# Optimization experiments

Hardware: AMD Instinct MI355X
Metric: run time of the kernel (lower is better)

The kernel has to match this reference:

```python
import jax, jax.numpy as jnp
import numpy as np

B, D, C = 16384, 1024, 2048

def setup_inputs() -> dict:
    key = jax.random.key(0)
    k1, k2 = jax.random.split(key)
    x = jax.random.normal(k1, (B, D), dtype=jnp.float32)
    # kaiming_normal_ with nonlinearity='relu': std = sqrt(2 / fan_in)
    W = jax.random.normal(k2, (C, D), dtype=jnp.float32) * jnp.sqrt(2.0 / D)
    return {"x": x, "W": W, "task_id": 0}

def reference(x, W, task_id):
    # Original: -(x[:, :, None] - W.T[None, :, :])**2 .mean(1)  -> [B, C]
    # Algebraic rewrite: -(||x||^2/D - 2*x.W^T/D + ||w||^2/D)
    d = jnp.asarray(x.shape[1], x.dtype)
    x2 = jnp.sum(x * x, axis=1, keepdims=True) / d          # [B, 1]
    w2 = jnp.sum(W * W, axis=1) / d                          # [C]
    cross = jnp.einsum('bd,cd->bc', x, W) * (2.0 / d)        # [B, C]
    return cross - x2 - w2[None, :]
```

## Files before the change

kernel.cpp:

```cpp
#include <hip/hip_runtime.h>
#include <hip/hip_bf16.h>
#include <stdint.h>

#define B_ROWS 16384
#define D_DIM  1024
#define C_DIM  2048
#define MT_TOT (B_ROWS / 16)
#define NT_TOT (C_DIM  / 16)
#define KT_TOT (D_DIM  / 32)

typedef short bf16x8 __attribute__((ext_vector_type(8)));
typedef float f32x4  __attribute__((ext_vector_type(4)));

__global__ __launch_bounds__(256) void pack_norm(
        const float* __restrict__ x, const float* __restrict__ W,
        ushort* __restrict__ Apk, ushort* __restrict__ Bpk,
        float* __restrict__ x2, float* __restrict__ w2) {
    int chunk = blockIdx.x * 4 + (threadIdx.x >> 6);
    const int lane = threadIdx.x & 63;
    const int XCH = MT_TOT * KT_TOT;
    const float* src; ushort* dst; float* norm;
    if (chunk < XCH) { src = x; dst = Apk; norm = x2; }
    else             { src = W; dst = Bpk; norm = w2; chunk -= XCH; }
    const int tile = chunk >> 5;
    const int kt   = chunk & 31;

    const int row = tile * 16 + (lane & 15);
    const int k0  = kt * 32 + (lane >> 4) * 8;
    const float4 v0 = *(const float4*)(src + (size_t)row * D_DIM + k0);
    const float4 v1 = *(const float4*)(src + (size_t)row * D_DIM + k0 + 4);
    float s = v0.x*v0.x + v0.y*v0.y + v0.z*v0.z + v0.w*v0.w
            + v1.x*v1.x + v1.y*v1.y + v1.z*v1.z + v1.w*v1.w;

    ushort u[8]; __hip_bfloat16 h;
    h = __float2bfloat16(v0.x); u[0] = *(const ushort*)&h;
    h = __float2bfloat16(v0.y); u[1] = *(const ushort*)&h;
    h = __float2bfloat16(v0.z); u[2] = *(const ushort*)&h;
    h = __float2bfloat16(v0.w); u[3] = *(const ushort*)&h;
    h = __float2bfloat16(v1.x); u[4] = *(const ushort*)&h;
    h = __float2bfloat16(v1.y); u[5] = *(const ushort*)&h;
    h = __float2bfloat16(v1.z); u[6] = *(const ushort*)&h;
    h = __float2bfloat16(v1.w); u[7] = *(const ushort*)&h;
    *(bf16x8*)(dst + ((size_t)chunk * 64 + lane) * 8) = *(const bf16x8*)u;

    s += __shfl_xor(s, 16, 64);
    s += __shfl_xor(s, 32, 64);
    if (lane < 16) atomicAdd(norm + tile * 16 + lane, s * (1.0f / (float)D_DIM));
}

__global__ __launch_bounds__(256, 3) void gemm_pklds(
        const ushort* __restrict__ Apk, const ushort* __restrict__ Bpk,
        const float* __restrict__ x2, const float* __restrict__ w2,
        float* __restrict__ out) {
    __shared__ ushort As[16 * 512];
    __shared__ ushort Bs[16 * 512];

    const int tid  = threadIdx.x;
    const int lane = tid & 63;
    const int wv   = tid >> 6;

    const int wid = (blockIdx.x & 7) * 256 + (blockIdx.x >> 3);
    const int bm  = wid >> 4;
    const int bn  = wid & 15;

    const ushort* aSrc = Apk + ((size_t)(bm * 8) * KT_TOT) * 512 + lane * 8;
    const ushort* bSrc = Bpk + ((size_t)(bn * 8) * KT_TOT) * 512 + lane * 8;

    const ushort* aRd = As + (wv >> 1) * 4 * 1024 + lane * 8;
    const ushort* bRd = Bs + (wv & 1) * 4 * 1024 + lane * 8;

    f32x4 acc[4][4];
    #pragma unroll
    for (int mi = 0; mi < 4; ++mi)
        #pragma unroll
        for (int ni = 0; ni < 4; ++ni)
            acc[mi][ni] = (f32x4){0.f, 0.f, 0.f, 0.f};

    for (int kt = 0; kt < KT_TOT; kt += 2) {
        if (wv < 2) {
            #pragma unroll
            for (int r = 0; r < 8; ++r) {
                const int c    = wv * 8 + r;
                const int tile = c >> 1, ks = c & 1;
                __builtin_amdgcn_global_load_lds(
                    (const __attribute__((address_space(1))) void*)(
                        aSrc + ((size_t)tile * KT_TOT + kt + ks) * 512),
                    (__attribute__((address_space(3))) void*)(As + c * 512), 16, 0, 0);
            }
        } else {
            #pragma unroll
            for (int r = 0; r < 8; ++r) {
                const int c    = (wv - 2) * 8 + r;
                const int tile = c >> 1, ks = c & 1;
                __builtin_amdgcn_global_load_lds(
                    (const __attribute__((address_space(1))) void*)(
                        bSrc + ((size_t)tile * KT_TOT + kt + ks) * 512),
                    (__attribute__((address_space(3))) void*)(Bs + c * 512), 16, 0, 0);
            }
        }
        __syncthreads();

        #pragma unroll
        for (int ks = 0; ks < 2; ++ks) {
            bf16x8 a[4], b[4];
            #pragma unroll
            for (int mi = 0; mi < 4; ++mi)
                a[mi] = *(const bf16x8*)(aRd + mi * 1024 + ks * 512);
            #pragma unroll
            for (int ni = 0; ni < 4; ++ni)
                b[ni] = *(const bf16x8*)(bRd + ni * 1024 + ks * 512);
            #pragma unroll
            for (int mi = 0; mi < 4; ++mi)
                #pragma unroll
                for (int ni = 0; ni < 4; ++ni)
                    acc[mi][ni] = __builtin_amdgcn_mfma_f32_16x16x32_bf16(
                        a[mi], b[ni], acc[mi][ni], 0, 0, 0);
        }
        __syncthreads();
    }

    const float scale = 2.0f / (float)D_DIM;
    const int rsel = lane & 15;
    const int quad = lane >> 4;
    const int mT0  = bm * 8 + (wv >> 1) * 4;
    const int nT0  = bn * 8 + (wv & 1) * 4;
    const int row0 = mT0 * 16 + quad * 4;
    const int col0 = nT0 * 16 + rsel;

    float x2r[4][4];
    #pragma unroll
    for (int mi = 0; mi < 4; ++mi)
        #pragma unroll
        for (int r = 0; r < 4; ++r)
            x2r[mi][r] = x2[row0 + mi * 16 + r];

    #pragma unroll
    for (int ni = 0; ni < 4; ++ni) {
        const int c = col0 + ni * 16;
        const float wc = w2[c];
        #pragma unroll
        for (int mi = 0; mi < 4; ++mi) {
            #pragma unroll
            for (int r = 0; r < 4; ++r) {
                const int rr = row0 + mi * 16 + r;
                out[(size_t)rr * C_DIM + c] = acc[mi][ni][r] * scale - x2r[mi][r] - wc;
            }
        }
    }
}

extern "C" void kernel_launch(void* const* d_in, const int* in_sizes, int n_in,
                              void* d_out, int out_size, void* d_ws, size_t ws_size,
                              hipStream_t stream) {
    const float* x = (const float*)d_in[0];
    const float* W = (const float*)d_in[1];
    float* out = (float*)d_out;

    char* ws = (char*)d_ws;
    ushort* Apk = (ushort*)ws;
    ushort* Bpk = (ushort*)(ws + (size_t)B_ROWS * D_DIM * sizeof(ushort));
    float*  x2  = (float*)(ws + (size_t)(B_ROWS + C_DIM) * D_DIM * sizeof(ushort));
    float*  w2  = x2 + B_ROWS;

    hipMemsetAsync(x2, 0, (B_ROWS + C_DIM) * sizeof(float), stream);

    pack_norm<<<(MT_TOT * KT_TOT + NT_TOT * KT_TOT) / 4, 256, 0, stream>>>(
        x, W, Apk, Bpk, x2, w2);

    gemm_pklds<<<(B_ROWS / 128) * (C_DIM / 128), 256, 0, stream>>>(
        Apk, Bpk, x2, w2, out);
}
```

Measured before the change: 255.1 us.

## Rewrite GEMM as 256x256-tile, 8-wave kernel with phased double-buffered LDS pipeline

Replaces the 128x128-tile, 4-wave GEMM with a 256x256-tile, 512-thread kernel. Each wave now computes a 128x64 sub-tile. The K loop is split into four phases that interleave global-to-LDS prefetch of the next K slices with MFMA work on the current buffer. It uses explicit vmcnt waits, raw barriers and s_setprio to keep matrix instructions flowing. This aims to raise data reuse per LDS byte and hide memory latency, at the cost of more registers (32 accumulators per wave), 128KB of LDS and fragile hand-placed synchronisation.

Result: slower. 272.1 us (+6.6%).

```diff
diff --git a/kernel.cpp b/kernel.cpp
--- a/kernel.cpp
+++ b/kernel.cpp
@@ -5,12 +5,21 @@
 #define B_ROWS 16384
 #define D_DIM  1024
 #define C_DIM  2048
+#define KT32   (D_DIM / 32)
+#define KT     (D_DIM / 64)
 #define MT_TOT (B_ROWS / 16)
 #define NT_TOT (C_DIM  / 16)
-#define KT_TOT (D_DIM  / 32)
 
 typedef short bf16x8 __attribute__((ext_vector_type(8)));
 typedef float f32x4  __attribute__((ext_vector_type(4)));
+
+#define AS1 __attribute__((address_space(1)))
+#define AS3 __attribute__((address_space(3)))
+#define BARRIER __builtin_amdgcn_s_barrier()
+#define LGKM0 asm volatile("s_waitcnt lgkmcnt(0)")
+#define VMCNT(n) asm volatile("s_waitcnt vmcnt(" #n ")" ::: "memory")
+#define PRIO1 __builtin_amdgcn_s_setprio(1)
+#define PRIO0 __builtin_amdgcn_s_setprio(0)
 
 __global__ __launch_bounds__(256) void pack_norm(
         const float* __restrict__ x, const float* __restrict__ W,
@@ -18,7 +27,7 @@
         float* __restrict__ x2, float* __restrict__ w2) {
     int chunk = blockIdx.x * 4 + (threadIdx.x >> 6);
     const int lane = threadIdx.x & 63;
-    const int XCH = MT_TOT * KT_TOT;
+    const int XCH = MT_TOT * KT32;
     const float* src; ushort* dst; float* norm;
     if (chunk < XCH) { src = x; dst = Apk; norm = x2; }
     else             { src = W; dst = Bpk; norm = w2; chunk -= XCH; }
@@ -48,105 +57,131 @@
     if (lane < 16) atomicAdd(norm + tile * 16 + lane, s * (1.0f / (float)D_DIM));
 }
 
-__global__ __launch_bounds__(256, 3) void gemm_pklds(
+__global__ __launch_bounds__(512, 2) void gemm_8ph(
         const ushort* __restrict__ Apk, const ushort* __restrict__ Bpk,
         const float* __restrict__ x2, const float* __restrict__ w2,
         float* __restrict__ out) {
-    __shared__ ushort As[16 * 512];
-    __shared__ ushort Bs[16 * 512];
+    __shared__ ushort As[32768];
+    __shared__ ushort Bs[32768];
 
     const int tid  = threadIdx.x;
     const int lane = tid & 63;
     const int wv   = tid >> 6;
-
-    const int wid = (blockIdx.x & 7) * 256 + (blockIdx.x >> 3);
-    const int bm  = wid >> 4;
-    const int bn  = wid & 15;
-
-    const ushort* aSrc = Apk + ((size_t)(bm * 8) * KT_TOT) * 512 + lane * 8;
-    const ushort* bSrc = Bpk + ((size_t)(bn * 8) * KT_TOT) * 512 + lane * 8;
-
-    const ushort* aRd = As + (wv >> 1) * 4 * 1024 + lane * 8;
-    const ushort* bRd = Bs + (wv & 1) * 4 * 1024 + lane * 8;
-
-    f32x4 acc[4][4];
+    const int wm   = wv >> 2;
+    const int wn   = wv & 3;
+
+    const int wid = (blockIdx.x & 7) * 64 + (blockIdx.x >> 3);
+    const int bm  = wid >> 3;
+    const int bn  = wid & 7;
+
+    const ushort* aSrc = Apk + (size_t)bm * 16 * KT32 * 512 + lane * 8;
+    const ushort* bSrc = Bpk + (size_t)bn * 16 * KT32 * 512 + lane * 8;
+    const ushort* aRd  = As + wm * 8192 + lane * 8;
+    const ushort* bRd  = Bs + wn * 4096 + lane * 8;
+
+    const int mt0 = wv * 2, mt1 = wv * 2 + 1;
+
+#define STA(mt, ktc, ldsOff) __builtin_amdgcn_global_load_lds( \
+        (const AS1 void*)(aSrc + ((size_t)(mt) * KT32 + (ktc)) * 512), \
+        (AS3 void*)(As + (ldsOff)), 16, 0, 0)
+#define STB(nt, ktc, ldsOff) __builtin_amdgcn_global_load_lds( \
+        (const AS1 void*)(bSrc + ((size_t)(nt) * KT32 + (ktc)) * 512), \
+        (AS3 void*)(Bs + (ldsOff)), 16, 0, 0)
+#define LDA(bo, mi, ks) (*(const bf16x8*)(aRd + (bo) + (mi) * 1024 + (ks) * 512))
+#define LDB(bo, ni, ks) (*(const bf16x8*)(bRd + (bo) + (ni) * 1024 + (ks) * 512))
+#define MFMA4(av, mi) \
+    acc[mi][0] = __builtin_amdgcn_mfma_f32_16x16x32_bf16(av, b0, acc[mi][0], 0, 0, 0); \
+    acc[mi][1] = __builtin_amdgcn_mfma_f32_16x16x32_bf16(av, b1, acc[mi][1], 0, 0, 0); \
+    acc[mi][2] = __builtin_amdgcn_mfma_f32_16x16x32_bf16(av, b2, acc[mi][2], 0, 0, 0); \
+    acc[mi][3] = __builtin_amdgcn_mfma_f32_16x16x32_bf16(av, b3, acc[mi][3], 0, 0, 0)
+
+    f32x4 acc[8][4];
     #pragma unroll
-    for (int mi = 0; mi < 4; ++mi)
+    for (int mi = 0; mi < 8; ++mi)
         #pragma unroll
         for (int ni = 0; ni < 4; ++ni)
             acc[mi][ni] = (f32x4){0.f, 0.f, 0.f, 0.f};
 
-    for (int kt = 0; kt < KT_TOT; kt += 2) {
-        if (wv < 2) {
-            #pragma unroll
-            for (int r = 0; r < 8; ++r) {
-                const int c    = wv * 8 + r;
-                const int tile = c >> 1, ks = c & 1;
-                __builtin_amdgcn_global_load_lds(
-                    (const __attribute__((address_space(1))) void*)(
-                        aSrc + ((size_t)tile * KT_TOT + kt + ks) * 512),
-                    (__attribute__((address_space(3))) void*)(As + c * 512), 16, 0, 0);
-            }
-        } else {
-            #pragma unroll
-            for (int r = 0; r < 8; ++r) {
-                const int c    = (wv - 2) * 8 + r;
-                const int tile = c >> 1, ks = c & 1;
-                __builtin_amdgcn_global_load_lds(
-                    (const __attribute__((address_space(1))) void*)(
-                        bSrc + ((size_t)tile * KT_TOT + kt + ks) * 512),
-                    (__attribute__((address_space(3))) void*)(Bs + c * 512), 16, 0, 0);
-            }
-        }
-        __syncthreads();
-
-        #pragma unroll
-        for (int ks = 0; ks < 2; ++ks) {
-            bf16x8 a[4], b[4];
-            #pragma unroll
-            for (int mi = 0; mi < 4; ++mi)
-                a[mi] = *(const bf16x8*)(aRd + mi * 1024 + ks * 512);
-            #pragma unroll
-            for (int ni = 0; ni < 4; ++ni)
-                b[ni] = *(const bf16x8*)(bRd + ni * 1024 + ks * 512);
-            #pragma unroll
-            for (int mi = 0; mi < 4; ++mi)
-                #pragma unroll
-                for (int ni = 0; ni < 4; ++ni)
-                    acc[mi][ni] = __builtin_amdgcn_mfma_f32_16x16x32_bf16(
-                        a[mi], b[ni], acc[mi][ni], 0, 0, 0);
-        }
-        __syncthreads();
+    STA(mt0, 0, mt0 * 1024);              STA(mt1, 0, mt1 * 1024);
+    STB(mt0, 0, mt0 * 1024);              STB(mt1, 0, mt1 * 1024);
+    STA(mt0, 1, mt0 * 1024 + 512);        STA(mt1, 1, mt1 * 1024 + 512);
+    STB(mt0, 1, mt0 * 1024 + 512);        STB(mt1, 1, mt1 * 1024 + 512);
+    STA(mt0, 2, 16384 + mt0 * 1024);      STA(mt1, 2, 16384 + mt1 * 1024);
+    STB(mt0, 2, 16384 + mt0 * 1024);      STB(mt1, 2, 16384 + mt1 * 1024);
+    VMCNT(8);
+    BARRIER;
+
+    #pragma unroll 2
+    for (int kt = 0; kt < KT; ++kt) {
+        const int bo  = (kt & 1) * 16384;
+        const int nbo = bo ^ 16384;
+        const int kc1 = ((kt + 1) * 2 + 1) & 31;
+        const int kc2 = ((kt + 2) * 2) & 31;
+        bf16x8 a0, a1, a2, a3, b0, b1, b2, b3;
+
+        b0 = LDB(bo, 0, 0); b1 = LDB(bo, 1, 0); b2 = LDB(bo, 2, 0); b3 = LDB(bo, 3, 0);
+        a0 = LDA(bo, 0, 0); a1 = LDA(bo, 1, 0); a2 = LDA(bo, 2, 0); a3 = LDA(bo, 3, 0);
+        STA(mt0, kc1, nbo + mt0 * 1024 + 512);
+        STA(mt1, kc1, nbo + mt1 * 1024 + 512);
+        BARRIER; LGKM0; PRIO1;
+        MFMA4(a0, 0); MFMA4(a1, 1); MFMA4(a2, 2); MFMA4(a3, 3);
+        PRIO0; BARRIER;
+
+        a0 = LDA(bo, 4, 0); a1 = LDA(bo, 5, 0); a2 = LDA(bo, 6, 0); a3 = LDA(bo, 7, 0);
+        STB(mt0, kc1, nbo + mt0 * 1024 + 512);
+        STB(mt1, kc1, nbo + mt1 * 1024 + 512);
+        VMCNT(8);
+        BARRIER; LGKM0; PRIO1;
+        MFMA4(a0, 4); MFMA4(a1, 5); MFMA4(a2, 6); MFMA4(a3, 7);
+        PRIO0; BARRIER;
+
+        b0 = LDB(bo, 0, 1); b1 = LDB(bo, 1, 1); b2 = LDB(bo, 2, 1); b3 = LDB(bo, 3, 1);
+        a0 = LDA(bo, 0, 1); a1 = LDA(bo, 1, 1); a2 = LDA(bo, 2, 1); a3 = LDA(bo, 3, 1);
+        STA(mt0, kc2, bo + mt0 * 1024);
+        STA(mt1, kc2, bo + mt1 * 1024);
+        BARRIER; LGKM0; PRIO1;
+        MFMA4(a0, 0); MFMA4(a1, 1); MFMA4(a2, 2); MFMA4(a3, 3);
+        PRIO0; BARRIER;
+
+        a0 = LDA(bo, 4, 1); a1 = LDA(bo, 5, 1); a2 = LDA(bo, 6, 1); a3 = LDA(bo, 7, 1);
+        STB(mt0, kc2, bo + mt0 * 1024);
+        STB(mt1, kc2, bo + mt1 * 1024);
+        VMCNT(8);
+        BARRIER; LGKM0; PRIO1;
+        MFMA4(a0, 4); MFMA4(a1, 5); MFMA4(a2, 6); MFMA4(a3, 7);
+        PRIO0; BARRIER;
     }
 
     const float scale = 2.0f / (float)D_DIM;
     const int rsel = lane & 15;
     const int quad = lane >> 4;
-    const int mT0  = bm * 8 + (wv >> 1) * 4;
-    const int nT0  = bn * 8 + (wv & 1) * 4;
-    const int row0 = mT0 * 16 + quad * 4;
-    const int col0 = nT0 * 16 + rsel;
-
-    float x2r[4][4];
+    const int row0 = bm * 256 + wm * 128 + quad * 4;
+    const int col0 = bn * 256 + wn * 64 + rsel;
+
+    float w2c[4];
     #pragma unroll
-    for (int mi = 0; mi < 4; ++mi)
+    for (int ni = 0; ni < 4; ++ni) w2c[ni] = w2[col0 + ni * 16];
+
+    #pragma unroll
+    for (int mi = 0; mi < 8; ++mi) {
+        const int rbase = row0 + mi * 16;
+        float xr[4];
         #pragma unroll
-        for (int r = 0; r < 4; ++r)
-            x2r[mi][r] = x2[row0 + mi * 16 + r];
-
-    #pragma unroll
-    for (int ni = 0; ni < 4; ++ni) {
-        const int c = col0 + ni * 16;
-        const float wc = w2[c];
+        for (int r = 0; r < 4; ++r) xr[r] = x2[rbase + r];
         #pragma unroll
-        for (int mi = 0; mi < 4; ++mi) {
+        for (int ni = 0; ni < 4; ++ni) {
+            const int c = col0 + ni * 16;
             #pragma unroll
-            for (int r = 0; r < 4; ++r) {
-                const int rr = row0 + mi * 16 + r;
-                out[(size_t)rr * C_DIM + c] = acc[mi][ni][r] * scale - x2r[mi][r] - wc;
-            }
+            for (int r = 0; r < 4; ++r)
+                out[(size_t)(rbase + r) * C_DIM + c] =
+                    acc[mi][ni][r] * scale - xr[r] - w2c[ni];
         }
     }
+#undef STA
+#undef STB
+#undef LDA
+#undef LDB
+#undef MFMA4
 }
 
 extern "C" void kernel_launch(void* const* d_in, const int* in_sizes, int n_in,
@@ -164,9 +199,9 @@
 
     hipMemsetAsync(x2, 0, (B_ROWS + C_DIM) * sizeof(float), stream);
 
-    pack_norm<<<(MT_TOT * KT_TOT + NT_TOT * KT_TOT) / 4, 256, 0, stream>>>(
+    pack_norm<<<(MT_TOT * KT32 + NT_TOT * KT32) / 4, 256, 0, stream>>>(
         x, W, Apk, Bpk, x2, w2);
 
-    gemm_pklds<<<(B_ROWS / 128) * (C_DIM / 128), 256, 0, stream>>>(
+    gemm_8ph<<<(B_ROWS / 256) * (C_DIM / 256), 512, 0, stream>>>(
         Apk, Bpk, x2, w2, out);
 }
```

## Triple-buffer LDS staging with async prefetch two K-steps ahead

Applied to the files above, without the earlier changes.

Replaces the load-all-then-compute loop, which had two full syncthreads per double K-step, with a 3-stage LDS ring buffer. Each iteration issues global_load_lds for step kt+2 while computing step kt, and uses explicit vmcnt waits and raw barriers instead of __syncthreads. MFMA blocks run at raised wave priority. The goal is to hide global-to-LDS latency behind compute. The cost is a wasted wraparound prefetch at the tail and reliance on hand-placed waitcnt correctness.

New measurement: 245.8 us. 1.04x faster.

```diff
diff --git a/kernel.cpp b/kernel.cpp
--- a/kernel.cpp
+++ b/kernel.cpp
@@ -5,12 +5,20 @@
 #define B_ROWS 16384
 #define D_DIM  1024
 #define C_DIM  2048
+#define KT32   (D_DIM / 32)
 #define MT_TOT (B_ROWS / 16)
 #define NT_TOT (C_DIM  / 16)
-#define KT_TOT (D_DIM  / 32)
 
 typedef short bf16x8 __attribute__((ext_vector_type(8)));
 typedef float f32x4  __attribute__((ext_vector_type(4)));
+
+#define AS1 __attribute__((address_space(1)))
+#define AS3 __attribute__((address_space(3)))
+#define BARRIER __builtin_amdgcn_s_barrier()
+#define LGKM0 asm volatile("s_waitcnt lgkmcnt(0)")
+#define VMCNT(n) asm volatile("s_waitcnt vmcnt(" #n ")" ::: "memory")
+#define PRIO1 __builtin_amdgcn_s_setprio(1)
+#define PRIO0 __builtin_amdgcn_s_setprio(0)
 
 __global__ __launch_bounds__(256) void pack_norm(
         const float* __restrict__ x, const float* __restrict__ W,
@@ -18,7 +26,7 @@
         float* __restrict__ x2, float* __restrict__ w2) {
     int chunk = blockIdx.x * 4 + (threadIdx.x >> 6);
     const int lane = threadIdx.x & 63;
-    const int XCH = MT_TOT * KT_TOT;
+    const int XCH = MT_TOT * KT32;
     const float* src; ushort* dst; float* norm;
     if (chunk < XCH) { src = x; dst = Apk; norm = x2; }
     else             { src = W; dst = Bpk; norm = w2; chunk -= XCH; }
@@ -48,12 +56,12 @@
     if (lane < 16) atomicAdd(norm + tile * 16 + lane, s * (1.0f / (float)D_DIM));
 }
 
-__global__ __launch_bounds__(256, 3) void gemm_pklds(
+__global__ __launch_bounds__(256, 3) void gemm_tb(
         const ushort* __restrict__ Apk, const ushort* __restrict__ Bpk,
         const float* __restrict__ x2, const float* __restrict__ w2,
         float* __restrict__ out) {
-    __shared__ ushort As[16 * 512];
-    __shared__ ushort Bs[16 * 512];
+    __shared__ ushort As[3 * 4096];
+    __shared__ ushort Bs[3 * 4096];
 
     const int tid  = threadIdx.x;
     const int lane = tid & 63;
@@ -63,11 +71,28 @@
     const int bm  = wid >> 4;
     const int bn  = wid & 15;
 
-    const ushort* aSrc = Apk + ((size_t)(bm * 8) * KT_TOT) * 512 + lane * 8;
-    const ushort* bSrc = Bpk + ((size_t)(bn * 8) * KT_TOT) * 512 + lane * 8;
+    const ushort* aSrc = Apk + ((size_t)(bm * 8) * KT32) * 512 + lane * 8;
+    const ushort* bSrc = Bpk + ((size_t)(bn * 8) * KT32) * 512 + lane * 8;
 
-    const ushort* aRd = As + (wv >> 1) * 4 * 1024 + lane * 8;
-    const ushort* bRd = Bs + (wv & 1) * 4 * 1024 + lane * 8;
+    const ushort* aRd = As + (wv >> 1) * 2048 + lane * 8;
+    const ushort* bRd = Bs + (wv & 1) * 2048 + lane * 8;
+
+    const int t0 = wv, t1 = wv + 4;
+
+#define STAGE(ktc, bufO) do { \
+    __builtin_amdgcn_global_load_lds( \
+        (const AS1 void*)(aSrc + ((size_t)t0 * KT32 + (ktc)) * 512), \
+        (AS3 void*)(As + (bufO) + t0 * 512), 16, 0, 0); \
+    __builtin_amdgcn_global_load_lds( \
+        (const AS1 void*)(aSrc + ((size_t)t1 * KT32 + (ktc)) * 512), \
+        (AS3 void*)(As + (bufO) + t1 * 512), 16, 0, 0); \
+    __builtin_amdgcn_global_load_lds( \
+        (const AS1 void*)(bSrc + ((size_t)t0 * KT32 + (ktc)) * 512), \
+        (AS3 void*)(Bs + (bufO) + t0 * 512), 16, 0, 0); \
+    __builtin_amdgcn_global_load_lds( \
+        (const AS1 void*)(bSrc + ((size_t)t1 * KT32 + (ktc)) * 512), \
+        (AS3 void*)(Bs + (bufO) + t1 * 512), 16, 0, 0); \
+  } while (0)
 
     f32x4 acc[4][4];
     #pragma unroll
@@ -76,47 +101,37 @@
         for (int ni = 0; ni < 4; ++ni)
             acc[mi][ni] = (f32x4){0.f, 0.f, 0.f, 0.f};
 
-    for (int kt = 0; kt < KT_TOT; kt += 2) {
-        if (wv < 2) {
-            #pragma unroll
-            for (int r = 0; r < 8; ++r) {
-                const int c    = wv * 8 + r;
-                const int tile = c >> 1, ks = c & 1;
-                __builtin_amdgcn_global_load_lds(
-                    (const __attribute__((address_space(1))) void*)(
-                        aSrc + ((size_t)tile * KT_TOT + kt + ks) * 512),
-                    (__attribute__((address_space(3))) void*)(As + c * 512), 16, 0, 0);
-            }
-        } else {
-            #pragma unroll
-            for (int r = 0; r < 8; ++r) {
-                const int c    = (wv - 2) * 8 + r;
-                const int tile = c >> 1, ks = c & 1;
-                __builtin_amdgcn_global_load_lds(
-                    (const __attribute__((address_space(1))) void*)(
-                        bSrc + ((size_t)tile * KT_TOT + kt + ks) * 512),
-                    (__attribute__((address_space(3))) void*)(Bs + c * 512), 16, 0, 0);
-            }
-        }
-        __syncthreads();
+    STAGE(0, 0);
+    STAGE(1, 4096);
+    VMCNT(4);
+    BARRIER;
 
+    int curO = 0, nxtO = 4096, stgO = 8192;
+    for (int kt = 0; kt < KT32; ++kt) {
+        bf16x8 a[4], b[4];
         #pragma unroll
-        for (int ks = 0; ks < 2; ++ks) {
-            bf16x8 a[4], b[4];
-            #pragma unroll
-            for (int mi = 0; mi < 4; ++mi)
-                a[mi] = *(const bf16x8*)(aRd + mi * 1024 + ks * 512);
+        for (int mi = 0; mi < 4; ++mi)
+            a[mi] = *(const bf16x8*)(aRd + curO + mi * 512);
+        #pragma unroll
+        for (int ni = 0; ni < 4; ++ni)
+            b[ni] = *(const bf16x8*)(bRd + curO + ni * 512);
+
+        STAGE((kt + 2) & 31, stgO);
+
+        VMCNT(4);
+        BARRIER;
+        LGKM0;
+        PRIO1;
+        #pragma unroll
+        for (int mi = 0; mi < 4; ++mi)
             #pragma unroll
             for (int ni = 0; ni < 4; ++ni)
-                b[ni] = *(const bf16x8*)(bRd + ni * 1024 + ks * 512);
-            #pragma unroll
-            for (int mi = 0; mi < 4; ++mi)
-                #pragma unroll
-                for (int ni = 0; ni < 4; ++ni)
-                    acc[mi][ni] = __builtin_amdgcn_mfma_f32_16x16x32_bf16(
-                        a[mi], b[ni], acc[mi][ni], 0, 0, 0);
-        }
-        __syncthreads();
+                acc[mi][ni] = __builtin_amdgcn_mfma_f32_16x16x32_bf16(
+                    a[mi], b[ni], acc[mi][ni], 0, 0, 0);
+        PRIO0;
+        BARRIER;
+
+        const int t = curO; curO = nxtO; nxtO = stgO; stgO = t;
     }
 
     const float scale = 2.0f / (float)D_DIM;
@@ -147,6 +162,7 @@
             }
         }
     }
+#undef STAGE
 }
 
 extern "C" void kernel_launch(void* const* d_in, const int* in_sizes, int n_in,
@@ -164,9 +180,9 @@
 
     hipMemsetAsync(x2, 0, (B_ROWS + C_DIM) * sizeof(float), stream);
 
-    pack_norm<<<(MT_TOT * KT_TOT + NT_TOT * KT_TOT) / 4, 256, 0, stream>>>(
+    pack_norm<<<(MT_TOT * KT32 + NT_TOT * KT32) / 4, 256, 0, stream>>>(
         x, W, Apk, Bpk, x2, w2);
 
-    gemm_pklds<<<(B_ROWS / 128) * (C_DIM / 128), 256, 0, stream>>>(
+    gemm_tb<<<(B_ROWS / 128) * (C_DIM / 128), 256, 0, stream>>>(
         Apk, Bpk, x2, w2, out);
 }
```

## Fuse fp32-to-bf16 packing and norms into a register-prefetched double-buffered GEMM

Applied to the files above, without the earlier changes.

Removes the separate pack/norm kernel and the memset. The GEMM now reads fp32 x and W directly, converts them to bf16 in registers and writes them into double-buffered LDS. The next K-slice is prefetched into registers while MFMAs run at raised wave priority, and the row norms are accumulated in registers and reduced in shared memory. This drops the extra launches and the bf16 workspace round trip. In exchange each block rereads fp32 inputs (twice the bytes of bf16) and recomputes norms redundantly across the 16 column blocks, and register pressure rises.

Result: slower. 396.7 us (+55.5%).

```diff
diff --git a/kernel.cpp b/kernel.cpp
--- a/kernel.cpp
+++ b/kernel.cpp
@@ -5,55 +5,38 @@
 #define B_ROWS 16384
 #define D_DIM  1024
 #define C_DIM  2048
-#define MT_TOT (B_ROWS / 16)
-#define NT_TOT (C_DIM  / 16)
-#define KT_TOT (D_DIM  / 32)
+#define KT32   32
 
 typedef short bf16x8 __attribute__((ext_vector_type(8)));
 typedef float f32x4  __attribute__((ext_vector_type(4)));
 
-__global__ __launch_bounds__(256) void pack_norm(
-        const float* __restrict__ x, const float* __restrict__ W,
-        ushort* __restrict__ Apk, ushort* __restrict__ Bpk,
-        float* __restrict__ x2, float* __restrict__ w2) {
-    int chunk = blockIdx.x * 4 + (threadIdx.x >> 6);
-    const int lane = threadIdx.x & 63;
-    const int XCH = MT_TOT * KT_TOT;
-    const float* src; ushort* dst; float* norm;
-    if (chunk < XCH) { src = x; dst = Apk; norm = x2; }
-    else             { src = W; dst = Bpk; norm = w2; chunk -= XCH; }
-    const int tile = chunk >> 5;
-    const int kt   = chunk & 31;
+#define PRIO1 __builtin_amdgcn_s_setprio(1)
+#define PRIO0 __builtin_amdgcn_s_setprio(0)
 
-    const int row = tile * 16 + (lane & 15);
-    const int k0  = kt * 32 + (lane >> 4) * 8;
-    const float4 v0 = *(const float4*)(src + (size_t)row * D_DIM + k0);
-    const float4 v1 = *(const float4*)(src + (size_t)row * D_DIM + k0 + 4);
-    float s = v0.x*v0.x + v0.y*v0.y + v0.z*v0.z + v0.w*v0.w
-            + v1.x*v1.x + v1.y*v1.y + v1.z*v1.z + v1.w*v1.w;
-
-    ushort u[8]; __hip_bfloat16 h;
-    h = __float2bfloat16(v0.x); u[0] = *(const ushort*)&h;
-    h = __float2bfloat16(v0.y); u[1] = *(const ushort*)&h;
-    h = __float2bfloat16(v0.z); u[2] = *(const ushort*)&h;
-    h = __float2bfloat16(v0.w); u[3] = *(const ushort*)&h;
-    h = __float2bfloat16(v1.x); u[4] = *(const ushort*)&h;
-    h = __float2bfloat16(v1.y); u[5] = *(const ushort*)&h;
-    h = __float2bfloat16(v1.z); u[6] = *(const ushort*)&h;
-    h = __float2bfloat16(v1.w); u[7] = *(const ushort*)&h;
-    *(bf16x8*)(dst + ((size_t)chunk * 64 + lane) * 8) = *(const bf16x8*)u;
-
-    s += __shfl_xor(s, 16, 64);
-    s += __shfl_xor(s, 32, 64);
-    if (lane < 16) atomicAdd(norm + tile * 16 + lane, s * (1.0f / (float)D_DIM));
+__device__ __forceinline__ float sq4(f32x4 v) {
+    return v[0]*v[0] + v[1]*v[1] + v[2]*v[2] + v[3]*v[3];
 }
 
-__global__ __launch_bounds__(256, 3) void gemm_pklds(
-        const ushort* __restrict__ Apk, const ushort* __restrict__ Bpk,
-        const float* __restrict__ x2, const float* __restrict__ w2,
+__device__ __forceinline__ void pk8(ushort* dst, f32x4 lo, f32x4 hi) {
+    ushort u[8]; __hip_bfloat16 h;
+    h = __float2bfloat16(lo[0]); u[0] = *(const ushort*)&h;
+    h = __float2bfloat16(lo[1]); u[1] = *(const ushort*)&h;
+    h = __float2bfloat16(lo[2]); u[2] = *(const ushort*)&h;
+    h = __float2bfloat16(lo[3]); u[3] = *(const ushort*)&h;
+    h = __float2bfloat16(hi[0]); u[4] = *(const ushort*)&h;
+    h = __float2bfloat16(hi[1]); u[5] = *(const ushort*)&h;
+    h = __float2bfloat16(hi[2]); u[6] = *(const ushort*)&h;
+    h = __float2bfloat16(hi[3]); u[7] = *(const ushort*)&h;
+    *(bf16x8*)dst = *(const bf16x8*)u;
+}
+
+__global__ __launch_bounds__(256, 3) void gemm_fused(
+        const float* __restrict__ x, const float* __restrict__ Wm,
         float* __restrict__ out) {
-    __shared__ ushort As[16 * 512];
-    __shared__ ushort Bs[16 * 512];
+    __shared__ ushort As[2 * 4096];
+    __shared__ ushort Bs[2 * 4096];
+    __shared__ float  nx[128];
+    __shared__ float  nw[128];
 
     const int tid  = threadIdx.x;
     const int lane = tid & 63;
@@ -63,11 +46,41 @@
     const int bm  = wid >> 4;
     const int bn  = wid & 15;
 
-    const ushort* aSrc = Apk + ((size_t)(bm * 8) * KT_TOT) * 512 + lane * 8;
-    const ushort* bSrc = Bpk + ((size_t)(bn * 8) * KT_TOT) * 512 + lane * 8;
+    const int r16 = lane & 15;
+    const int q   = lane >> 4;
 
-    const ushort* aRd = As + (wv >> 1) * 4 * 1024 + lane * 8;
-    const ushort* bRd = Bs + (wv & 1) * 4 * 1024 + lane * 8;
+    const float* pa0 = x  + ((size_t)(bm * 128 + wv * 16       + r16)) * D_DIM + q * 8;
+    const float* pa1 = x  + ((size_t)(bm * 128 + (wv + 4) * 16 + r16)) * D_DIM + q * 8;
+    const float* pb0 = Wm + ((size_t)(bn * 128 + wv * 16       + r16)) * D_DIM + q * 8;
+    const float* pb1 = Wm + ((size_t)(bn * 128 + (wv + 4) * 16 + r16)) * D_DIM + q * 8;
+
+    ushort* wA0 = As + wv * 512       + lane * 8;
+    ushort* wA1 = As + (wv + 4) * 512 + lane * 8;
+    ushort* wB0 = Bs + wv * 512       + lane * 8;
+    ushort* wB1 = Bs + (wv + 4) * 512 + lane * 8;
+
+    const ushort* aRd = As + (wv >> 1) * 2048 + lane * 8;
+    const ushort* bRd = Bs + (wv & 1) * 2048 + lane * 8;
+
+    float na0 = 0.f, na1 = 0.f, nb0 = 0.f, nb1 = 0.f;
+    f32x4 A0l, A0h, A1l, A1h, B0l, B0h, B1l, B1h;
+
+#define LOADK(kt) do { const int o_ = (kt) * 32;                  \
+    A0l = *(const f32x4*)(pa0 + o_); A0h = *(const f32x4*)(pa0 + o_ + 4); \
+    A1l = *(const f32x4*)(pa1 + o_); A1h = *(const f32x4*)(pa1 + o_ + 4); \
+    B0l = *(const f32x4*)(pb0 + o_); B0h = *(const f32x4*)(pb0 + o_ + 4); \
+    B1l = *(const f32x4*)(pb1 + o_); B1h = *(const f32x4*)(pb1 + o_ + 4); \
+  } while (0)
+
+#define NORMACC() do {                                            \
+    na0 += sq4(A0l) + sq4(A0h); na1 += sq4(A1l) + sq4(A1h);       \
+    nb0 += sq4(B0l) + sq4(B0h); nb1 += sq4(B1l) + sq4(B1h);       \
+  } while (0)
+
+#define CVTSTORE(bufO) do {                                       \
+    pk8(wA0 + (bufO), A0l, A0h); pk8(wA1 + (bufO), A1l, A1h);     \
+    pk8(wB0 + (bufO), B0l, B0h); pk8(wB1 + (bufO), B1l, B1h);     \
+  } while (0)
 
     f32x4 acc[4][4];
     #pragma unroll
@@ -76,68 +89,72 @@
         for (int ni = 0; ni < 4; ++ni)
             acc[mi][ni] = (f32x4){0.f, 0.f, 0.f, 0.f};
 
-    for (int kt = 0; kt < KT_TOT; kt += 2) {
-        if (wv < 2) {
-            #pragma unroll
-            for (int r = 0; r < 8; ++r) {
-                const int c    = wv * 8 + r;
-                const int tile = c >> 1, ks = c & 1;
-                __builtin_amdgcn_global_load_lds(
-                    (const __attribute__((address_space(1))) void*)(
-                        aSrc + ((size_t)tile * KT_TOT + kt + ks) * 512),
-                    (__attribute__((address_space(3))) void*)(As + c * 512), 16, 0, 0);
-            }
-        } else {
-            #pragma unroll
-            for (int r = 0; r < 8; ++r) {
-                const int c    = (wv - 2) * 8 + r;
-                const int tile = c >> 1, ks = c & 1;
-                __builtin_amdgcn_global_load_lds(
-                    (const __attribute__((address_space(1))) void*)(
-                        bSrc + ((size_t)tile * KT_TOT + kt + ks) * 512),
-                    (__attribute__((address_space(3))) void*)(Bs + c * 512), 16, 0, 0);
-            }
-        }
-        __syncthreads();
+    LOADK(0);
+    NORMACC();
+    CVTSTORE(0);
+    __syncthreads();
 
+    #pragma unroll 2
+    for (int kt = 0; kt < KT32; ++kt) {
+        const int cur = (kt & 1) * 4096;
+        const int nxt = cur ^ 4096;
+
+        bf16x8 a[4], b[4];
         #pragma unroll
-        for (int ks = 0; ks < 2; ++ks) {
-            bf16x8 a[4], b[4];
-            #pragma unroll
-            for (int mi = 0; mi < 4; ++mi)
-                a[mi] = *(const bf16x8*)(aRd + mi * 1024 + ks * 512);
+        for (int mi = 0; mi < 4; ++mi)
+            a[mi] = *(const bf16x8*)(aRd + cur + mi * 512);
+        #pragma unroll
+        for (int ni = 0; ni < 4; ++ni)
+            b[ni] = *(const bf16x8*)(bRd + cur + ni * 512);
+
+        LOADK((kt + 1) & 31);
+
+        PRIO1;
+        #pragma unroll
+        for (int mi = 0; mi < 4; ++mi)
             #pragma unroll
             for (int ni = 0; ni < 4; ++ni)
-                b[ni] = *(const bf16x8*)(bRd + ni * 1024 + ks * 512);
-            #pragma unroll
-            for (int mi = 0; mi < 4; ++mi)
-                #pragma unroll
-                for (int ni = 0; ni < 4; ++ni)
-                    acc[mi][ni] = __builtin_amdgcn_mfma_f32_16x16x32_bf16(
-                        a[mi], b[ni], acc[mi][ni], 0, 0, 0);
-        }
+                acc[mi][ni] = __builtin_amdgcn_mfma_f32_16x16x32_bf16(
+                    a[mi], b[ni], acc[mi][ni], 0, 0, 0);
+        PRIO0;
+
+        if (kt != 31) NORMACC();
+        CVTSTORE(nxt);
         __syncthreads();
     }
+
+    const float inv = 1.0f / (float)D_DIM;
+    float s0 = na0 * inv; s0 += __shfl_xor(s0, 16, 64); s0 += __shfl_xor(s0, 32, 64);
+    float s1 = na1 * inv; s1 += __shfl_xor(s1, 16, 64); s1 += __shfl_xor(s1, 32, 64);
+    float s2 = nb0 * inv; s2 += __shfl_xor(s2, 16, 64); s2 += __shfl_xor(s2, 32, 64);
+    float s3 = nb1 * inv; s3 += __shfl_xor(s3, 16, 64); s3 += __shfl_xor(s3, 32, 64);
+    if (lane < 16) {
+        nx[wv * 16 + lane]       = s0;
+        nx[(wv + 4) * 16 + lane] = s1;
+        nw[wv * 16 + lane]       = s2;
+        nw[(wv + 4) * 16 + lane] = s3;
+    }
+    __syncthreads();
 
     const float scale = 2.0f / (float)D_DIM;
     const int rsel = lane & 15;
     const int quad = lane >> 4;
-    const int mT0  = bm * 8 + (wv >> 1) * 4;
-    const int nT0  = bn * 8 + (wv & 1) * 4;
-    const int row0 = mT0 * 16 + quad * 4;
-    const int col0 = nT0 * 16 + rsel;
+    const int lr0  = (wv >> 1) * 64 + quad * 4;
+    const int lc0  = (wv & 1) * 64 + rsel;
+    const int row0 = bm * 128 + lr0;
+    const int col0 = bn * 128 + lc0;
 
     float x2r[4][4];
     #pragma unroll
     for (int mi = 0; mi < 4; ++mi)
         #pragma unroll
         for (int r = 0; r < 4; ++r)
-            x2r[mi][r] = x2[row0 + mi * 16 + r];
+            x2r[mi][r] = nx[lr0 + mi * 16 + r];
 
     #pragma unroll
     for (int ni = 0; ni < 4; ++ni) {
-        const int c = col0 + ni * 16;
-        const float wc = w2[c];
+        const int c  = col0 + ni * 16;
+        const float wc = nw[lc0 + ni * 16];
         #pragma unroll
         for (int mi = 0; mi < 4; ++mi) {
             #pragma unroll
@@ -147,6 +164,9 @@
             }
         }
     }
+#undef LOADK
+#undef NORMACC
+#undef CVTSTORE
 }
 
 extern "C" void kernel_launch(void* const* d_in, const int* in_sizes, int n_in,
@@ -155,18 +175,7 @@
     const float* x = (const float*)d_in[0];
     const float* W = (const float*)d_in[1];
     float* out = (float*)d_out;
+    (void)d_ws; (void)ws_size;
 
-    char* ws = (char*)d_ws;
-    ushort* Apk = (ushort*)ws;
-    ushort* Bpk = (ushort*)(ws + (size_t)B_ROWS * D_DIM * sizeof(ushort));
-    float*  x2  = (float*)(ws + (size_t)(B_ROWS + C_DIM) * D_DIM * sizeof(ushort));
-    float*  w2  = x2 + B_ROWS;
-
-    hipMemsetAsync(x2, 0, (B_ROWS + C_DIM) * sizeof(float), stream);
-
-    pack_norm<<<(MT_TOT * KT_TOT + NT_TOT * KT_TOT) / 4, 256, 0, stream>>>(
-        x, W, Apk, Bpk, x2, w2);
-
-    gemm_pklds<<<(B_ROWS / 128) * (C_DIM / 128), 256, 0, stream>>>(
-        Apk, Bpk, x2, w2, out);
+    gemm_fused<<<(B_ROWS / 128) * (C_DIM / 128), 256, 0, stream>>>(x, W, out);
 }
```
